# Optimization experiments

Hardware: AMD Instinct MI355X
Metric: run time of the kernel (lower is better)

The kernel has to match this reference:

```python
import jax, jax.numpy as jnp
import numpy as np

NUMS = 2048
DIM = 128

def setup_inputs() -> dict:
    key = jax.random.key(0)
    k1, k2 = jax.random.split(key)
    data = jax.random.normal(k1, (32, 512, DIM), dtype=jnp.float32)
    stdv = 1.0 / np.sqrt(DIM)
    weight = jax.random.uniform(k2, (NUMS, DIM), dtype=jnp.float32, minval=-stdv, maxval=stdv)
    return {"data": data, "weight": weight}

def reference(data, weight):
    b, t, d = data.shape
    nums = weight.shape[0]
    # attention scores: [b, t, nums]
    attention = jax.nn.sigmoid(jnp.einsum('btd,kd->btk', data, weight) / jnp.sqrt(jnp.asarray(d, data.dtype)))
    k_top = nums // 16 + 1  # 129
    topk_vals, _ = jax.lax.top_k(attention, k_top)  # [b, t, k_top]
    temporal_att = topk_vals.mean(axis=-1)          # [b, t]
    half = b // 2
    augment = jnp.einsum('btk,kd->btd', attention[:half], weight)  # [b//2, t, d]
    read_query = jnp.concatenate((data[:half], augment), axis=-1)  # [b//2, t, 2d]
    mem_score = 1.0 - temporal_att
    return (mem_score, read_query)
```

## Files before the change

### kernel.cpp

```cpp
#include <hip/hip_runtime.h>

typedef unsigned short u16;
typedef unsigned int u32;
typedef unsigned long long u64;
typedef __attribute__((ext_vector_type(8))) short short8;
typedef __attribute__((ext_vector_type(4))) float floatx4;

#define NUMS 2048
#define DIM 128
#define ROWS_TOT 16384
#define HALF_ROWS 8192
#define KTOP 129
#define MTILE 16
#define SCALE 0.08838834764831845f

__device__ __forceinline__ u16 f2bf(float f) {
  u32 u = __builtin_bit_cast(u32, f);
  u += 0x7FFFu + ((u >> 16) & 1u);
  return (u16)(u >> 16);
}
__device__ __forceinline__ float bf2f(u32 b) {
  return __builtin_bit_cast(float, b << 16);
}

__device__ __forceinline__ short8 pack_bf8(float4 a, float4 b) {
  short8 v;
  v[0] = (short)f2bf(a.x); v[1] = (short)f2bf(a.y);
  v[2] = (short)f2bf(a.z); v[3] = (short)f2bf(a.w);
  v[4] = (short)f2bf(b.x); v[5] = (short)f2bf(b.y);
  v[6] = (short)f2bf(b.z); v[7] = (short)f2bf(b.w);
  return v;
}

__global__ void cvt_w_k(const float* __restrict__ w, u16* __restrict__ wb,
                        u16* __restrict__ wt) {
  __shared__ u16 tile[32][33];
  const int tx = threadIdx.x, ty = threadIdx.y;
  const int x = blockIdx.x * 32 + tx;
  const int y0 = blockIdx.y * 32;
#pragma unroll
  for (int j = 0; j < 32; j += 8) {
    const u16 v = f2bf(w[(size_t)(y0 + ty + j) * DIM + x]);
    wb[(size_t)(y0 + ty + j) * DIM + x] = v;
    tile[ty + j][tx] = v;
  }
  __syncthreads();
  const int x2 = y0 + tx;
  const int y2 = blockIdx.x * 32 + ty;
#pragma unroll
  for (int j = 0; j < 32; j += 8)
    wt[(size_t)(y2 + j) * NUMS + x2] = tile[tx][ty + j];
}

__device__ __forceinline__ int s_idx(int r, int c) {
  return r * NUMS + ((((c >> 3) ^ r) << 3) | (c & 7));
}

__global__ __launch_bounds__(512, 4)
void fused_k(const float* __restrict__ dataF, const u16* __restrict__ wb,
             const u16* __restrict__ wt, float* __restrict__ out) {
  __shared__ u16 S[MTILE * NUMS];
  const int tid = threadIdx.x;
  const int r0 = blockIdx.x * MTILE;
  const int lane = tid & 63;
  const int wave = tid >> 6;
  const int m = lane & 15;
  const int quad = lane >> 4;

  short8 afrag[4];
  {
    const float* ap = dataF + (size_t)(r0 + m) * DIM + quad * 8;
#pragma unroll
    for (int ks = 0; ks < 4; ks++) {
      const float4 x = *(const float4*)(ap + ks * 32);
      const float4 y = *(const float4*)(ap + ks * 32 + 4);
      afrag[ks] = pack_bf8(x, y);
    }
  }
#pragma unroll 4
  for (int nt = 0; nt < 16; nt++) {
    const int n0 = wave * 256 + nt * 16;
    const u16* bp = wb + (size_t)(n0 + m) * DIM + quad * 8;
    floatx4 acc = {0.f, 0.f, 0.f, 0.f};
#pragma unroll
    for (int ks = 0; ks < 4; ks++) {
      short8 bfrag = *(const short8*)(bp + ks * 32);
      acc = __builtin_amdgcn_mfma_f32_16x16x32_bf16(afrag[ks], bfrag, acc, 0, 0, 0);
    }
    const int c = n0 + m;
#pragma unroll
    for (int reg = 0; reg < 4; reg++) {
      const int rr = quad * 4 + reg;
      float att = 1.f / (1.f + __expf(-acc[reg] * SCALE));
      att = fminf(fmaxf(att, 0.f), 1.f);
      S[s_idx(rr, c)] = f2bf(att);
    }
  }
  __syncthreads();

  if (r0 < HALF_ROWS) {
    {
      const int row = tid >> 5;
      const int c4 = (tid & 31) << 2;
      *(float4*)(out + 16384 + (size_t)(r0 + row) * 256 + c4) =
          *(const float4*)(dataF + (size_t)(r0 + row) * DIM + c4);
    }
    const int n0 = wave * 16;
    floatx4 acc = {0.f, 0.f, 0.f, 0.f};
    const u16* w0 = wt + (size_t)(n0 + m) * NUMS + quad * 8;
#pragma unroll 8
    for (int ks = 0; ks < 64; ks++) {
      const int chunk = ks * 4 + quad;
      short8 af = *(const short8*)(S + m * NUMS + ((chunk ^ m) << 3));
      short8 b0 = *(const short8*)(w0 + ks * 32);
      acc = __builtin_amdgcn_mfma_f32_16x16x32_bf16(af, b0, acc, 0, 0, 0);
    }
#pragma unroll
    for (int reg = 0; reg < 4; reg++) {
      const int row = quad * 4 + reg;
      out[16384 + (size_t)(r0 + row) * 256 + 128 + n0 + m] = acc[reg];
    }
  }

#pragma unroll
  for (int rv = 0; rv < 2; rv++) {
    const int rr = wave * 2 + rv;
    u32 bits[32];
#pragma unroll
    for (int j = 0; j < 4; j++) {
      const short8 v = *(const short8*)(S + rr * NUMS + (j * 64 + lane) * 8);
#pragma unroll
      for (int t = 0; t < 8; t++) bits[j * 8 + t] = (u32)(u16)v[t];
    }

    auto count_ge = [&](u32 t) -> int {
      int c = 0;
#pragma unroll
      for (int i = 0; i < 32; i++)
        c += __popcll(__ballot(bits[i] >= t));
      return c;
    };

    int cnt[8];
#pragma unroll
    for (int j = 0; j < 8; j++) cnt[j] = count_ge(0x3EE0u + ((u32)j << 4));
    u32 lo = 0u, hi = 0x3F81u;
#pragma unroll
    for (int j = 0; j < 8; j++)
      if (cnt[j] >= KTOP) lo = 0x3EE0u + ((u32)j << 4);
#pragma unroll
    for (int j = 7; j >= 0; j--)
      if (cnt[j] < KTOP) hi = 0x3EE0u + ((u32)j << 4);

    while (hi - lo > 1u) {
      const u32 mid = (lo + hi) >> 1;
      if (count_ge(mid) >= KTOP) lo = mid; else hi = mid;
    }
    const float vstar = bf2f(lo);

    float s = 0.f;
    int cgt = 0;
#pragma unroll
    for (int i = 0; i < 32; i++) {
      if (bits[i] > lo) s += bf2f(bits[i]);
      cgt += __popcll(__ballot(bits[i] > lo));
    }
#pragma unroll
    for (int off = 1; off < 64; off <<= 1) s += __shfl_xor(s, off);
    if (lane == 0) {
      const float mean = (s + (float)(KTOP - cgt) * vstar) * (1.f / (float)KTOP);
      out[r0 + rr] = 1.f - mean;
    }
  }
}

extern "C" void kernel_launch(void* const* d_in, const int* in_sizes, int n_in,
                              void* d_out, int out_size, void* d_ws, size_t ws_size,
                              hipStream_t stream) {
  const float* data = (const float*)d_in[0];
  const float* weight = (const float*)d_in[1];
  float* out = (float*)d_out;

  u16* wt = (u16*)d_ws;
  u16* wb = wt + NUMS * DIM;

  cvt_w_k<<<dim3(DIM / 32, NUMS / 32), dim3(32, 8), 0, stream>>>(weight, wb, wt);
  fused_k<<<dim3(ROWS_TOT / MTILE), dim3(512), 0, stream>>>(data, wb, wt, out);
}
```

Measured before the change: 167.8 us.

## Swap MFMA operands, pad LDS rows, and use SWAR per-lane top-k counting

The first GEMM now passes weights as the A operand and data as B, so each lane gets four consecutive columns and writes them to LDS as one packed 8-byte store into padded rows instead of XOR-swizzled scalar stores. The second GEMM is transposed the same way, so each lane writes a float4 of output. The top-k threshold search counts packed pairs of bf16 values with a SWAR subtract-and-mask popcount per lane, then reduces the counts across the wave with packed shuffles instead of ballots. It tries the eight candidate thresholds 0x3F00..0x3F07 first and only falls back to a full binary search when the answer lies outside that range. The fast path assumes the threshold usually lands in that narrow band, and the sigmoid clamp was dropped.

```diff
diff --git a/kernel.cpp b/kernel.cpp
--- a/kernel.cpp
+++ b/kernel.cpp
@@ -2,7 +2,6 @@
 
 typedef unsigned short u16;
 typedef unsigned int u32;
-typedef unsigned long long u64;
 typedef __attribute__((ext_vector_type(8))) short short8;
 typedef __attribute__((ext_vector_type(4))) float floatx4;
 
@@ -12,6 +11,7 @@
 #define HALF_ROWS 8192
 #define KTOP 129
 #define MTILE 16
+#define SP 2056
 #define SCALE 0.08838834764831845f
 
 __device__ __forceinline__ u16 f2bf(float f) {
@@ -21,15 +21,6 @@
 }
 __device__ __forceinline__ float bf2f(u32 b) {
   return __builtin_bit_cast(float, b << 16);
-}
-
-__device__ __forceinline__ short8 pack_bf8(float4 a, float4 b) {
-  short8 v;
-  v[0] = (short)f2bf(a.x); v[1] = (short)f2bf(a.y);
-  v[2] = (short)f2bf(a.z); v[3] = (short)f2bf(a.w);
-  v[4] = (short)f2bf(b.x); v[5] = (short)f2bf(b.y);
-  v[6] = (short)f2bf(b.z); v[7] = (short)f2bf(b.w);
-  return v;
 }
 
 __global__ void cvt_w_k(const float* __restrict__ w, u16* __restrict__ wb,
@@ -52,14 +43,10 @@
     wt[(size_t)(y2 + j) * NUMS + x2] = tile[tx][ty + j];
 }
 
-__device__ __forceinline__ int s_idx(int r, int c) {
-  return r * NUMS + ((((c >> 3) ^ r) << 3) | (c & 7));
-}
-
 __global__ __launch_bounds__(512, 4)
 void fused_k(const float* __restrict__ dataF, const u16* __restrict__ wb,
              const u16* __restrict__ wt, float* __restrict__ out) {
-  __shared__ u16 S[MTILE * NUMS];
+  __shared__ u16 S[MTILE * SP];
   const int tid = threadIdx.x;
   const int r0 = blockIdx.x * MTILE;
   const int lane = tid & 63;
@@ -67,34 +54,41 @@
   const int m = lane & 15;
   const int quad = lane >> 4;
 
-  short8 afrag[4];
+  short8 dfrag[4];
   {
     const float* ap = dataF + (size_t)(r0 + m) * DIM + quad * 8;
 #pragma unroll
     for (int ks = 0; ks < 4; ks++) {
       const float4 x = *(const float4*)(ap + ks * 32);
       const float4 y = *(const float4*)(ap + ks * 32 + 4);
-      afrag[ks] = pack_bf8(x, y);
-    }
-  }
+      short8 v;
+      v[0] = (short)f2bf(x.x); v[1] = (short)f2bf(x.y);
+      v[2] = (short)f2bf(x.z); v[3] = (short)f2bf(x.w);
+      v[4] = (short)f2bf(y.x); v[5] = (short)f2bf(y.y);
+      v[6] = (short)f2bf(y.z); v[7] = (short)f2bf(y.w);
+      dfrag[ks] = v;
+    }
+  }
+
+  u16* sbase = S + m * SP + wave * 256 + quad * 4;
 #pragma unroll 4
   for (int nt = 0; nt < 16; nt++) {
     const int n0 = wave * 256 + nt * 16;
-    const u16* bp = wb + (size_t)(n0 + m) * DIM + quad * 8;
+    const u16* wp = wb + (size_t)(n0 + m) * DIM + quad * 8;
     floatx4 acc = {0.f, 0.f, 0.f, 0.f};
 #pragma unroll
     for (int ks = 0; ks < 4; ks++) {
-      short8 bfrag = *(const short8*)(bp + ks * 32);
-      acc = __builtin_amdgcn_mfma_f32_16x16x32_bf16(afrag[ks], bfrag, acc, 0, 0, 0);
-    }
-    const int c = n0 + m;
-#pragma unroll
-    for (int reg = 0; reg < 4; reg++) {
-      const int rr = quad * 4 + reg;
-      float att = 1.f / (1.f + __expf(-acc[reg] * SCALE));
-      att = fminf(fmaxf(att, 0.f), 1.f);
-      S[s_idx(rr, c)] = f2bf(att);
-    }
+      const short8 wfrag = *(const short8*)(wp + ks * 32);
+      acc = __builtin_amdgcn_mfma_f32_16x16x32_bf16(wfrag, dfrag[ks], acc, 0, 0, 0);
+    }
+    float a0 = 1.f / (1.f + __expf(-acc[0] * SCALE));
+    float a1 = 1.f / (1.f + __expf(-acc[1] * SCALE));
+    float a2 = 1.f / (1.f + __expf(-acc[2] * SCALE));
+    float a3 = 1.f / (1.f + __expf(-acc[3] * SCALE));
+    uint2 p;
+    p.x = (u32)f2bf(a0) | ((u32)f2bf(a1) << 16);
+    p.y = (u32)f2bf(a2) | ((u32)f2bf(a3) << 16);
+    *(uint2*)(sbase + nt * 16) = p;
   }
   __syncthreads();
 
@@ -106,64 +100,94 @@
           *(const float4*)(dataF + (size_t)(r0 + row) * DIM + c4);
     }
     const int n0 = wave * 16;
+    const u16* wtp = wt + (size_t)(n0 + m) * NUMS + quad * 8;
+    const u16* sp2 = S + m * SP + quad * 8;
     floatx4 acc = {0.f, 0.f, 0.f, 0.f};
-    const u16* w0 = wt + (size_t)(n0 + m) * NUMS + quad * 8;
 #pragma unroll 8
     for (int ks = 0; ks < 64; ks++) {
-      const int chunk = ks * 4 + quad;
-      short8 af = *(const short8*)(S + m * NUMS + ((chunk ^ m) << 3));
-      short8 b0 = *(const short8*)(w0 + ks * 32);
-      acc = __builtin_amdgcn_mfma_f32_16x16x32_bf16(af, b0, acc, 0, 0, 0);
-    }
-#pragma unroll
-    for (int reg = 0; reg < 4; reg++) {
-      const int row = quad * 4 + reg;
-      out[16384 + (size_t)(r0 + row) * 256 + 128 + n0 + m] = acc[reg];
-    }
+      const short8 a = *(const short8*)(wtp + ks * 32);
+      const short8 b = *(const short8*)(sp2 + ks * 32);
+      acc = __builtin_amdgcn_mfma_f32_16x16x32_bf16(a, b, acc, 0, 0, 0);
+    }
+    float4 st;
+    st.x = acc[0]; st.y = acc[1]; st.z = acc[2]; st.w = acc[3];
+    *(float4*)(out + 16384 + (size_t)(r0 + m) * 256 + 128 + n0 + quad * 4) = st;
   }
 
 #pragma unroll
   for (int rv = 0; rv < 2; rv++) {
     const int rr = wave * 2 + rv;
-    u32 bits[32];
+    const u16* rp = S + rr * SP + lane * 8;
+    u32 x[16], xh[16];
 #pragma unroll
     for (int j = 0; j < 4; j++) {
-      const short8 v = *(const short8*)(S + rr * NUMS + (j * 64 + lane) * 8);
-#pragma unroll
-      for (int t = 0; t < 8; t++) bits[j * 8 + t] = (u32)(u16)v[t];
-    }
-
-    auto count_ge = [&](u32 t) -> int {
+      const short8 v = *(const short8*)(rp + j * 512);
+      const u32* pv = (const u32*)&v;
+      x[j * 4 + 0] = pv[0]; x[j * 4 + 1] = pv[1];
+      x[j * 4 + 2] = pv[2]; x[j * 4 + 3] = pv[3];
+    }
+#pragma unroll
+    for (int i = 0; i < 16; i++) xh[i] = x[i] | 0x80008000u;
+
+    auto cnt_ge = [&](u32 t) -> int {
+      const u32 t2 = t * 0x10001u;
       int c = 0;
 #pragma unroll
-      for (int i = 0; i < 32; i++)
-        c += __popcll(__ballot(bits[i] >= t));
+      for (int i = 0; i < 16; i++)
+        c += __popc((xh[i] - t2) & 0x80008000u);
       return c;
     };
 
-    int cnt[8];
-#pragma unroll
-    for (int j = 0; j < 8; j++) cnt[j] = count_ge(0x3EE0u + ((u32)j << 4));
-    u32 lo = 0u, hi = 0x3F81u;
-#pragma unroll
-    for (int j = 0; j < 8; j++)
-      if (cnt[j] >= KTOP) lo = 0x3EE0u + ((u32)j << 4);
-#pragma unroll
-    for (int j = 7; j >= 0; j--)
-      if (cnt[j] < KTOP) hi = 0x3EE0u + ((u32)j << 4);
-
-    while (hi - lo > 1u) {
-      const u32 mid = (lo + hi) >> 1;
-      if (count_ge(mid) >= KTOP) lo = mid; else hi = mid;
-    }
+    int c8[8];
+#pragma unroll
+    for (int j = 0; j < 8; j++) c8[j] = cnt_ge(0x3F00u + (u32)j);
+    u32 pk[4];
+#pragma unroll
+    for (int j = 0; j < 4; j++) pk[j] = (u32)c8[2 * j] | ((u32)c8[2 * j + 1] << 16);
+#pragma unroll
+    for (int off = 1; off < 64; off <<= 1) {
+#pragma unroll
+      for (int j = 0; j < 4; j++) pk[j] += __shfl_xor(pk[j], off);
+    }
+    int cw[8];
+#pragma unroll
+    for (int j = 0; j < 4; j++) {
+      cw[2 * j] = (int)(pk[j] & 0xFFFFu);
+      cw[2 * j + 1] = (int)(pk[j] >> 16);
+    }
+
+    u32 lo;
+    int cgt;
+    if (cw[0] >= KTOP && cw[7] < KTOP) {
+      int idx = 0;
+#pragma unroll
+      for (int j = 1; j < 8; j++) idx += (cw[j] >= KTOP) ? 1 : 0;
+      lo = 0x3F00u + (u32)idx;
+      cgt = cw[idx + 1];
+    } else {
+      u32 L = 0u, H = 0x3F81u;
+      while (H - L > 1u) {
+        const u32 mid = (L + H) >> 1;
+        int cc = cnt_ge(mid);
+#pragma unroll
+        for (int off = 1; off < 64; off <<= 1) cc += __shfl_xor(cc, off);
+        if (cc >= KTOP) L = mid; else H = mid;
+      }
+      lo = L;
+      int cg = cnt_ge(lo + 1);
+#pragma unroll
+      for (int off = 1; off < 64; off <<= 1) cg += __shfl_xor(cg, off);
+      cgt = cg;
+    }
+
     const float vstar = bf2f(lo);
-
     float s = 0.f;
-    int cgt = 0;
-#pragma unroll
-    for (int i = 0; i < 32; i++) {
-      if (bits[i] > lo) s += bf2f(bits[i]);
-      cgt += __popcll(__ballot(bits[i] > lo));
+#pragma unroll
+    for (int i = 0; i < 16; i++) {
+      const float v0 = bf2f(x[i] & 0xFFFFu);
+      const float v1 = __builtin_bit_cast(float, x[i] & 0xFFFF0000u);
+      if (v0 > vstar) s += v0;
+      if (v1 > vstar) s += v1;
     }
 #pragma unroll
     for (int off = 1; off < 64; off <<= 1) s += __shfl_xor(s, off);
```

New measurement: 162.1 us. 3.4% less time.
